# Optimization experiments

Measured on AMD Instinct MI355X. Metric: run time of the kernel, lower is better.

The kernel has to match this reference:

```python
import jax, jax.numpy as jnp
import numpy as np
from jax import lax

D_MODEL = 1024
D_STATE = 16


def setup_inputs() -> dict:
    key = jax.random.key(0)
    ks = jax.random.split(key, 7)
    B, L = 4, 2048
    x = jax.random.normal(ks[0], (B, L, D_MODEL), dtype=jnp.float32)
    s = 1.0 / np.sqrt(D_MODEL)
    W_dt = jax.random.uniform(ks[1], (D_MODEL, D_MODEL), jnp.float32, -s, s)
    b_dt = jax.random.uniform(ks[2], (D_MODEL,), jnp.float32, -s, s)
    W_B = jax.random.uniform(ks[3], (D_STATE, D_MODEL), jnp.float32, -s, s)
    W_C = jax.random.uniform(ks[4], (D_STATE, D_MODEL), jnp.float32, -s, s)
    A = jax.random.normal(ks[5], (D_MODEL, D_STATE), dtype=jnp.float32)
    A_log = jnp.log(jnp.abs(A) + 1e-4)
    D = jnp.ones((D_MODEL,), dtype=jnp.float32)
    return {"x": x, "W_dt": W_dt, "b_dt": b_dt, "W_B": W_B, "W_C": W_C,
            "A_log": A_log, "D": D}


def reference(x, W_dt, b_dt, W_B, W_C, A_log, D):
    B, L, Dm = x.shape
    N = A_log.shape[1]
    dt = jax.nn.softplus(jnp.einsum('bld,ed->ble', x, W_dt) + b_dt)  # [B,L,D]
    Bp = jnp.einsum('bld,nd->bln', x, W_B)   # [B,L,N]
    Cp = jnp.einsum('bld,nd->bln', x, W_C)   # [B,L,N]
    A = -jnp.exp(A_log)                      # [D,N]
    dA = jnp.exp(dt[..., None] * A)          # [B,L,D,N]
    # fuse dB * x: dB[bldn] = dt*Bp; input term = dB * x
    dBx = dt[..., None] * Bp[:, :, None, :] * x[..., None]  # [B,L,D,N]

    def step(h, inp):
        dA_t, dBx_t, C_t, x_t = inp
        h = dA_t * h + dBx_t                              # [B,D,N]
        y = jnp.einsum('bdn,bn->bd', h, C_t) + D * x_t    # [B,D]
        return h, y

    h0 = jnp.zeros((B, Dm, N), dtype=x.dtype)
    xs = (jnp.swapaxes(dA, 0, 1), jnp.swapaxes(dBx, 0, 1),
          jnp.swapaxes(Cp, 0, 1), jnp.swapaxes(x, 0, 1))
    _, ys = lax.scan(step, h0, xs)           # ys: [L,B,D]
    return jnp.swapaxes(ys, 0, 1)            # [B,L,D]
```

## Files before the change

### kernel.cpp

```cpp
#include <hip/hip_runtime.h>
#include <hip/hip_bf16.h>
#include <math.h>

#define DM 1024
#define DS 16
#define BB 4
#define LL 2048
#define LC 32
#define NC (LL/LC)
#define MT 8192
#define NT64 16
#define NCT 17

typedef __attribute__((ext_vector_type(8))) short short8;
typedef __attribute__((ext_vector_type(4))) short short4v;
typedef __attribute__((ext_vector_type(4))) float floatx4;

__device__ __forceinline__ float softplus_fast(float v) {
  return fmaxf(v, 0.f) + __logf(1.f + __expf(-fabsf(v)));
}
__device__ __forceinline__ float bf2f(short s) {
  union { short s2[2]; float f; } u; u.s2[0] = 0; u.s2[1] = s; return u.f;
}

__global__ __launch_bounds__(256) void convert_kernel(
    const float* __restrict__ X, const float* __restrict__ W_dt,
    const float* __restrict__ WB, const float* __restrict__ WC,
    __hip_bfloat16* __restrict__ Xb, __hip_bfloat16* __restrict__ XbT,
    __hip_bfloat16* __restrict__ Wx)
{
  const int tid = threadIdx.x;
  if (blockIdx.x < 2048) {
    __shared__ __hip_bfloat16 tile[64 * 65];
    const int tb = blockIdx.x;
    const int t0 = (tb & 127) * 64;
    const int d0 = (tb >> 7) * 64;
    const int tr  = tid >> 4;
    const int tc4 = (tid & 15) * 4;
#pragma unroll
    for (int p = 0; p < 4; ++p) {
      const int row = p * 16 + tr;
      const float4 v = *(const float4*)&X[(size_t)(t0 + row) * DM + d0 + tc4];
      union { short4v v4; __hip_bfloat16 h[4]; } pk;
      pk.h[0] = __float2bfloat16(v.x); pk.h[1] = __float2bfloat16(v.y);
      pk.h[2] = __float2bfloat16(v.z); pk.h[3] = __float2bfloat16(v.w);
      tile[row * 65 + tc4 + 0] = pk.h[0];
      tile[row * 65 + tc4 + 1] = pk.h[1];
      tile[row * 65 + tc4 + 2] = pk.h[2];
      tile[row * 65 + tc4 + 3] = pk.h[3];
      *(short4v*)&Xb[(size_t)(t0 + row) * DM + d0 + tc4] = pk.v4;
    }
    __syncthreads();
#pragma unroll
    for (int p = 0; p < 4; ++p) {
      const int drow = p * 16 + tr;
      union { short4v v4; __hip_bfloat16 h[4]; } pk;
#pragma unroll
      for (int q = 0; q < 4; ++q)
        pk.h[q] = tile[(tc4 + q) * 65 + drow];
      *(short4v*)&XbT[(size_t)(d0 + drow) * MT + t0 + tc4] = pk.v4;
    }
    return;
  }
  const size_t u0 = (size_t)(blockIdx.x - 2048) * 256 + tid;
  const size_t NW = (size_t)DM * DM / 8;
  const size_t NB = (size_t)DS * DM / 8;
  const float* src;
  __hip_bfloat16* dst;
  size_t u;
  if (u0 < NW)           { src = W_dt; dst = Wx;                       u = u0; }
  else if (u0 < NW + NB) { src = WB;   dst = Wx + (size_t)1024 * DM;   u = u0 - NW; }
  else if (u0 < NW + 2 * NB) { src = WC; dst = Wx + (size_t)1040 * DM; u = u0 - NW - NB; }
  else {
    const size_t z = u0 - NW - 2 * NB;
    const short8 zz = {0, 0, 0, 0, 0, 0, 0, 0};
    *(short8*)&Wx[(size_t)1056 * DM + z * 8] = zz;
    return;
  }
  const float4 a = *(const float4*)&src[u * 8];
  const float4 b = *(const float4*)&src[u * 8 + 4];
  union { short8 v; __hip_bfloat16 h[8]; } o;
  o.h[0] = __float2bfloat16(a.x); o.h[1] = __float2bfloat16(a.y);
  o.h[2] = __float2bfloat16(a.z); o.h[3] = __float2bfloat16(a.w);
  o.h[4] = __float2bfloat16(b.x); o.h[5] = __float2bfloat16(b.y);
  o.h[6] = __float2bfloat16(b.z); o.h[7] = __float2bfloat16(b.w);
  *(short8*)&dst[u * 8] = o.v;
}

__global__ __launch_bounds__(512, 4) void gemm_dt_mfma(
    const __hip_bfloat16* __restrict__ Xb, const __hip_bfloat16* __restrict__ Wx,
    const float* __restrict__ bias, __hip_bfloat16* __restrict__ DTt,
    float* __restrict__ BP, float* __restrict__ CP)
{
  __shared__ short As[2][256 * 64];
  __shared__ short Bs[2][64 * 64];
  const int tid  = threadIdx.x;
  const int lane = tid & 63;
  const int wid  = tid >> 6;
  const int wm   = wid >> 1, wn = wid & 1;

  const int bid  = blockIdx.x;
  const int tile = (bid & 7) * 68 + (bid >> 3);
  const int row0 = (tile / NCT) * 256;
  const int col0 = (tile % NCT) * 64;

  const floatx4 zero = {0.f, 0.f, 0.f, 0.f};
  floatx4 acc[4][2];
#pragma unroll
  for (int i = 0; i < 4; ++i)
#pragma unroll
    for (int j = 0; j < 2; ++j) acc[i][j] = zero;

  auto STAGE = [&](int buf, int t) {
    const int k0 = t * 64;
#pragma unroll
    for (int q = 0; q < 4; ++q) {
      const int fe = q * 512 + tid;
      const int r  = fe >> 3;
      const int kk = (fe & 7) ^ (r & 7);
      __builtin_amdgcn_global_load_lds(
          (const __attribute__((address_space(1))) void*)&Xb[(size_t)(row0 + r) * DM + k0 + kk * 8],
          (__attribute__((address_space(3))) void*)&As[buf][fe * 8], 16, 0, 0);
    }
    {
      const int fe = tid;
      const int r  = fe >> 3;
      const int kk = (fe & 7) ^ (r & 7);
      __builtin_amdgcn_global_load_lds(
          (const __attribute__((address_space(1))) void*)&Wx[(size_t)(col0 + r) * DM + k0 + kk * 8],
          (__attribute__((address_space(3))) void*)&Bs[buf][fe * 8], 16, 0, 0);
    }
  };

  const int fr = lane & 15;
  const int ks = lane >> 4;

  STAGE(0, 0);
  int cur = 0;
  for (int t = 0; t < NT64; ++t) {
    if (t + 1 < NT64) {
      STAGE(cur ^ 1, t + 1);
      asm volatile("s_waitcnt vmcnt(5)" ::: "memory");
    } else {
      asm volatile("s_waitcnt vmcnt(0)" ::: "memory");
    }
    __builtin_amdgcn_s_barrier();
    __builtin_amdgcn_sched_barrier(0);

    short8 af[4][2], bfr[2][2];
#pragma unroll
    for (int i = 0; i < 4; ++i) {
      const int ar = wm * 64 + i * 16 + fr;
#pragma unroll
      for (int s = 0; s < 2; ++s) {
        const int ch = (ks + 4 * s) ^ (ar & 7);
        af[i][s] = *(const short8*)&As[cur][ar * 64 + ch * 8];
      }
    }
#pragma unroll
    for (int j = 0; j < 2; ++j) {
      const int br = wn * 32 + j * 16 + fr;
#pragma unroll
      for (int s = 0; s < 2; ++s) {
        const int ch = (ks + 4 * s) ^ (br & 7);
        bfr[j][s] = *(const short8*)&Bs[cur][br * 64 + ch * 8];
      }
    }
    __builtin_amdgcn_s_setprio(1);
#pragma unroll
    for (int s = 0; s < 2; ++s)
#pragma unroll
      for (int i = 0; i < 4; ++i)
#pragma unroll
        for (int j = 0; j < 2; ++j)
          acc[i][j] = __builtin_amdgcn_mfma_f32_16x16x32_bf16(af[i][s], bfr[j][s], acc[i][j], 0, 0, 0);
    __builtin_amdgcn_s_setprio(0);
    __builtin_amdgcn_sched_barrier(0);

    if (t + 1 < NT64) {
      __builtin_amdgcn_s_barrier();
      cur ^= 1;
    }
  }

  const int cl = lane & 15;
  const int rg = lane >> 4;
  if (col0 < 1024) {
#pragma unroll
    for (int i = 0; i < 4; ++i) {
      const size_t rowbase = (size_t)(row0 + wm * 64 + i * 16 + rg * 4);
#pragma unroll
      for (int j = 0; j < 2; ++j) {
        const int col = col0 + wn * 32 + j * 16 + cl;
        union { short4v v4; __hip_bfloat16 h[4]; } pk;
#pragma unroll
        for (int r = 0; r < 4; ++r)
          pk.h[r] = __float2bfloat16(softplus_fast(acc[i][j][r] + bias[col]));
        *(short4v*)&DTt[(size_t)col * MT + rowbase] = pk.v4;
      }
    }
  } else if (wn == 0) {
#pragma unroll
    for (int i = 0; i < 4; ++i) {
#pragma unroll
      for (int r = 0; r < 4; ++r) {
        const size_t row = (size_t)(row0 + wm * 64 + i * 16 + rg * 4 + r);
        BP[row * DS + cl] = acc[i][0][r];
        CP[row * DS + cl] = acc[i][1][r];
      }
    }
  }
}

__global__ __launch_bounds__(256) void scan_partial_kernel(
    const __hip_bfloat16* __restrict__ DTt, const __hip_bfloat16* __restrict__ XbT,
    const float* __restrict__ Bp, const float* __restrict__ A_log,
    float* __restrict__ SD, __hip_bfloat16* __restrict__ HP)
{
  __shared__ float sB[LC * DS];
  const int tid = threadIdx.x;
  const int d  = blockIdx.x * 128 + (tid >> 1);
  const int nh = tid & 1;
  const int c = blockIdx.y;
  const int b = blockIdx.z;
  const int l0 = c * LC;

  if (tid < LC * DS / 4)
    ((float4*)sB)[tid] = ((const float4*)&Bp[((size_t)b * LL + l0) * DS])[tid];

  float A[8], h[8];
  float sdt = 0.f;
  const float4* arow = (const float4*)&A_log[(size_t)d * DS + nh * 8];
  {
    const float4 a0 = arow[0], a1 = arow[1];
    A[0]=-__expf(a0.x); A[1]=-__expf(a0.y); A[2]=-__expf(a0.z); A[3]=-__expf(a0.w);
    A[4]=-__expf(a1.x); A[5]=-__expf(a1.y); A[6]=-__expf(a1.z); A[7]=-__expf(a1.w);
  }
#pragma unroll
  for (int n = 0; n < 8; ++n) h[n] = 0.f;

  const __hip_bfloat16* dT = &DTt[(size_t)d * MT + (size_t)b * LL + l0];
  const __hip_bfloat16* xT = &XbT[(size_t)d * MT + (size_t)b * LL + l0];
  short8 d8 = *(const short8*)dT;
  short8 x8 = *(const short8*)xT;
  __syncthreads();

  for (int l = 0; l < LC; l += 8) {
    short8 d8n, x8n;
    if (l + 8 < LC) {
      d8n = *(const short8*)(dT + l + 8);
      x8n = *(const short8*)(xT + l + 8);
    }
#pragma unroll
    for (int u = 0; u < 8; ++u) {
      const float dtv = bf2f(d8[u]), xv = bf2f(x8[u]);
      const float dx = dtv * xv;
      sdt += dtv;
      const float4 b0 = ((const float4*)sB)[(l+u)*4 + nh*2 + 0];
      const float4 b1 = ((const float4*)sB)[(l+u)*4 + nh*2 + 1];
      const float bb[8] = {b0.x,b0.y,b0.z,b0.w, b1.x,b1.y,b1.z,b1.w};
#pragma unroll
      for (int n = 0; n < 8; ++n) {
        const float dA = __expf(dtv * A[n]);
        h[n] = fmaf(dA, h[n], dx * bb[n]);
      }
    }
    d8 = d8n; x8 = x8n;
  }
  if (nh == 0) SD[((size_t)b * NC + c) * DM + d] = sdt;
  const size_t o = (((size_t)b * NC + c) * DM + d) * DS + nh * 8;
  union { short8 v; __hip_bfloat16 h[8]; } pk;
#pragma unroll
  for (int n = 0; n < 8; ++n) pk.h[n] = __float2bfloat16(h[n]);
  *(short8*)&HP[o] = pk.v;
}

__global__ __launch_bounds__(256) void combine_kernel(
    const float* __restrict__ SD, const float* __restrict__ A_log,
    __hip_bfloat16* HP)
{
  const int idx = blockIdx.x * 256 + threadIdx.x;
  const int b  = idx >> 14;
  const int dn = idx & 16383;
  const int d  = dn >> 4;
  const float A = -__expf(A_log[dn]);
  float h = 0.f;
#pragma unroll 4
  for (int c = 0; c < NC; ++c) {
    const size_t o = (((size_t)b * NC + c) << 14) + dn;
    const float p  = __expf(SD[((size_t)b * NC + c) * DM + d] * A);
    const float hp = __bfloat162float(HP[o]);
    HP[o] = __float2bfloat16(h);
    h = fmaf(p, h, hp);
  }
}

__global__ __launch_bounds__(256) void scan_final_kernel(
    const __hip_bfloat16* __restrict__ DTt, const __hip_bfloat16* __restrict__ XbT,
    const float* __restrict__ Bp, const float* __restrict__ Cp,
    const float* __restrict__ A_log, const float* __restrict__ Dvec,
    const __hip_bfloat16* __restrict__ Hin, float* __restrict__ Y)
{
  __shared__ float sB[LC * DS], sC[LC * DS];
  const int tid = threadIdx.x;
  const int d  = blockIdx.x * 128 + (tid >> 1);
  const int nh = tid & 1;
  const int c = blockIdx.y;
  const int b = blockIdx.z;
  const int l0 = c * LC;

  if (tid < 128)  ((float4*)sB)[tid] = ((const float4*)&Bp[((size_t)b * LL + l0) * DS])[tid];
  else            ((float4*)sC)[tid - 128] = ((const float4*)&Cp[((size_t)b * LL + l0) * DS])[tid - 128];

  float A[8], h[8];
  const float4* arow = (const float4*)&A_log[(size_t)d * DS + nh * 8];
  {
    const float4 a0 = arow[0], a1 = arow[1];
    A[0]=-__expf(a0.x); A[1]=-__expf(a0.y); A[2]=-__expf(a0.z); A[3]=-__expf(a0.w);
    A[4]=-__expf(a1.x); A[5]=-__expf(a1.y); A[6]=-__expf(a1.z); A[7]=-__expf(a1.w);
  }
  const size_t o = (((size_t)b * NC + c) * DM + d) * DS + nh * 8;
  {
    const short8 hv = *(const short8*)&Hin[o];
#pragma unroll
    for (int n = 0; n < 8; ++n) h[n] = bf2f(hv[n]);
  }
  const float Dd = Dvec[d];
  const size_t tok0 = (size_t)b * LL + l0;
  const __hip_bfloat16* dT = &DTt[(size_t)d * MT + tok0];
  const __hip_bfloat16* xT = &XbT[(size_t)d * MT + tok0];
  short8 d8 = *(const short8*)dT;
  short8 x8 = *(const short8*)xT;
  __syncthreads();

  for (int l = 0; l < LC; l += 8) {
    short8 d8n, x8n;
    if (l + 8 < LC) {
      d8n = *(const short8*)(dT + l + 8);
      x8n = *(const short8*)(xT + l + 8);
    }
#pragma unroll
    for (int u = 0; u < 8; ++u) {
      const float dtv = bf2f(d8[u]), xv = bf2f(x8[u]);
      const float dx = dtv * xv;
      const float4 b0 = ((const float4*)sB)[(l+u)*4 + nh*2 + 0];
      const float4 b1 = ((const float4*)sB)[(l+u)*4 + nh*2 + 1];
      const float bb[8] = {b0.x,b0.y,b0.z,b0.w, b1.x,b1.y,b1.z,b1.w};
      const float4 c0 = ((const float4*)sC)[(l+u)*4 + nh*2 + 0];
      const float4 c1 = ((const float4*)sC)[(l+u)*4 + nh*2 + 1];
      const float cc[8] = {c0.x,c0.y,c0.z,c0.w, c1.x,c1.y,c1.z,c1.w};
      float y = 0.f;
#pragma unroll
      for (int n = 0; n < 8; ++n) {
        const float dA = __expf(dtv * A[n]);
        h[n] = fmaf(dA, h[n], dx * bb[n]);
        y = fmaf(h[n], cc[n], y);
      }
      y += __shfl_xor(y, 1, 64);
      if (nh == 0) Y[(tok0 + l + u) * DM + d] = fmaf(Dd, xv, y);
    }
    d8 = d8n; x8 = x8n;
  }
}

extern "C" void kernel_launch(void* const* d_in, const int* in_sizes, int n_in,
                              void* d_out, int out_size, void* d_ws, size_t ws_size,
                              hipStream_t stream)
{
  const float* x     = (const float*)d_in[0];
  const float* W_dt  = (const float*)d_in[1];
  const float* b_dt  = (const float*)d_in[2];
  const float* W_B   = (const float*)d_in[3];
  const float* W_C   = (const float*)d_in[4];
  const float* A_log = (const float*)d_in[5];
  const float* Dv    = (const float*)d_in[6];
  float* Y  = (float*)d_out;
  float* ws = (float*)d_ws;

  __hip_bfloat16* DTt = (__hip_bfloat16*)ws;
  float* BP = ws + (size_t)MT * DM / 2;
  float* CP = BP + (size_t)MT * DS;
  __hip_bfloat16* Xb  = (__hip_bfloat16*)(CP + (size_t)MT * DS);
  __hip_bfloat16* XbT = Xb + (size_t)MT * DM;
  __hip_bfloat16* Wx  = XbT + (size_t)MT * DM;
  float* SD = (float*)(Wx + (size_t)1088 * DM);
  __hip_bfloat16* HP = (__hip_bfloat16*)(SD + (size_t)BB * NC * DM);

  convert_kernel<<<2592, 256, 0, stream>>>(x, W_dt, W_B, W_C, Xb, XbT, Wx);
  gemm_dt_mfma<<<544, 512, 0, stream>>>(Xb, Wx, b_dt, DTt, BP, CP);
  scan_partial_kernel<<<dim3(DM * 2 / 256, NC, BB), 256, 0, stream>>>(DTt, XbT, BP, A_log, SD, HP);
  combine_kernel<<<(BB * DM * DS) / 256, 256, 0, stream>>>(SD, A_log, HP);
  scan_final_kernel<<<dim3(DM * 2 / 256, NC, BB), 256, 0, stream>>>(DTt, XbT, BP, CP, A_log, Dv, HP, Y);
}
```

Baseline: 119.1 us.

## Fold B/C projection into dt GEMM tiles via split-K atomics

Removes the extra 17th column tile that computed the B and C projections. Each of the 16 dt column tiles now computes one 64-wide K-slice of the B/C projection using the A fragments it already holds, and accumulates the partial results into BP/CP with atomicAdd after a memset. This cuts the grid from 544 to 512 blocks so it matches the CU count more evenly, and drops the zero-padding work in the convert kernel. In exchange it adds a memset launch, many float atomics, and a non-deterministic summation order.

```diff
diff --git a/kernel.cpp b/kernel.cpp
--- a/kernel.cpp
+++ b/kernel.cpp
@@ -10,7 +10,6 @@
 #define NC (LL/LC)
 #define MT 8192
 #define NT64 16
-#define NCT 17
 
 typedef __attribute__((ext_vector_type(8))) short short8;
 typedef __attribute__((ext_vector_type(4))) short short4v;
@@ -68,15 +67,10 @@
   const float* src;
   __hip_bfloat16* dst;
   size_t u;
-  if (u0 < NW)           { src = W_dt; dst = Wx;                       u = u0; }
-  else if (u0 < NW + NB) { src = WB;   dst = Wx + (size_t)1024 * DM;   u = u0 - NW; }
-  else if (u0 < NW + 2 * NB) { src = WC; dst = Wx + (size_t)1040 * DM; u = u0 - NW - NB; }
-  else {
-    const size_t z = u0 - NW - 2 * NB;
-    const short8 zz = {0, 0, 0, 0, 0, 0, 0, 0};
-    *(short8*)&Wx[(size_t)1056 * DM + z * 8] = zz;
-    return;
-  }
+  if (u0 < NW)               { src = W_dt; dst = Wx;                       u = u0; }
+  else if (u0 < NW + NB)     { src = WB;   dst = Wx + (size_t)1024 * DM;   u = u0 - NW; }
+  else if (u0 < NW + 2 * NB) { src = WC;   dst = Wx + (size_t)1040 * DM;   u = u0 - NW - NB; }
+  else return;
   const float4 a = *(const float4*)&src[u * 8];
   const float4 b = *(const float4*)&src[u * 8 + 4];
   union { short8 v; __hip_bfloat16 h[8]; } o;
@@ -100,9 +94,10 @@
   const int wm   = wid >> 1, wn = wid & 1;
 
   const int bid  = blockIdx.x;
-  const int tile = (bid & 7) * 68 + (bid >> 3);
-  const int row0 = (tile / NCT) * 256;
-  const int col0 = (tile % NCT) * 64;
+  const int tile = (bid & 7) * 64 + (bid >> 3);
+  const int row0 = (tile >> 4) * 256;
+  const int ct   = tile & 15;
+  const int col0 = ct * 64;
 
   const floatx4 zero = {0.f, 0.f, 0.f, 0.f};
   floatx4 acc[4][2];
@@ -110,6 +105,9 @@
   for (int i = 0; i < 4; ++i)
 #pragma unroll
     for (int j = 0; j < 2; ++j) acc[i][j] = zero;
+  floatx4 acc_bc[4];
+#pragma unroll
+  for (int i = 0; i < 4; ++i) acc_bc[i] = zero;
 
   auto STAGE = [&](int buf, int t) {
     const int k0 = t * 64;
@@ -135,7 +133,13 @@
   const int fr = lane & 15;
   const int ks = lane >> 4;
 
+  const size_t bcrow = (size_t)(1024 + wn * 16 + fr) * DM + ct * 64 + ks * 8;
+  short8 bc0, bc1;
+
   STAGE(0, 0);
+  bc0 = *(const short8*)&Wx[bcrow];
+  bc1 = *(const short8*)&Wx[bcrow + 32];
+
   int cur = 0;
   for (int t = 0; t < NT64; ++t) {
     if (t + 1 < NT64) {
@@ -175,6 +179,13 @@
         for (int j = 0; j < 2; ++j)
           acc[i][j] = __builtin_amdgcn_mfma_f32_16x16x32_bf16(af[i][s], bfr[j][s], acc[i][j], 0, 0, 0);
     __builtin_amdgcn_s_setprio(0);
+    if (t == ct) {
+#pragma unroll
+      for (int i = 0; i < 4; ++i) {
+        acc_bc[i] = __builtin_amdgcn_mfma_f32_16x16x32_bf16(af[i][0], bc0, acc_bc[i], 0, 0, 0);
+        acc_bc[i] = __builtin_amdgcn_mfma_f32_16x16x32_bf16(af[i][1], bc1, acc_bc[i], 0, 0, 0);
+      }
+    }
     __builtin_amdgcn_sched_barrier(0);
 
     if (t + 1 < NT64) {
@@ -185,29 +196,26 @@
 
   const int cl = lane & 15;
   const int rg = lane >> 4;
-  if (col0 < 1024) {
-#pragma unroll
-    for (int i = 0; i < 4; ++i) {
-      const size_t rowbase = (size_t)(row0 + wm * 64 + i * 16 + rg * 4);
-#pragma unroll
-      for (int j = 0; j < 2; ++j) {
-        const int col = col0 + wn * 32 + j * 16 + cl;
-        union { short4v v4; __hip_bfloat16 h[4]; } pk;
-#pragma unroll
-        for (int r = 0; r < 4; ++r)
-          pk.h[r] = __float2bfloat16(softplus_fast(acc[i][j][r] + bias[col]));
-        *(short4v*)&DTt[(size_t)col * MT + rowbase] = pk.v4;
-      }
-    }
-  } else if (wn == 0) {
-#pragma unroll
-    for (int i = 0; i < 4; ++i) {
-#pragma unroll
-      for (int r = 0; r < 4; ++r) {
-        const size_t row = (size_t)(row0 + wm * 64 + i * 16 + rg * 4 + r);
-        BP[row * DS + cl] = acc[i][0][r];
-        CP[row * DS + cl] = acc[i][1][r];
-      }
+#pragma unroll
+  for (int i = 0; i < 4; ++i) {
+    const size_t rowbase = (size_t)(row0 + wm * 64 + i * 16 + rg * 4);
+#pragma unroll
+    for (int j = 0; j < 2; ++j) {
+      const int col = col0 + wn * 32 + j * 16 + cl;
+      union { short4v v4; __hip_bfloat16 h[4]; } pk;
+#pragma unroll
+      for (int r = 0; r < 4; ++r)
+        pk.h[r] = __float2bfloat16(softplus_fast(acc[i][j][r] + bias[col]));
+      *(short4v*)&DTt[(size_t)col * MT + rowbase] = pk.v4;
+    }
+  }
+  float* dstBC = (wn == 0) ? BP : CP;
+#pragma unroll
+  for (int i = 0; i < 4; ++i) {
+#pragma unroll
+    for (int r = 0; r < 4; ++r) {
+      const size_t row = (size_t)(row0 + wm * 64 + i * 16 + rg * 4 + r);
+      atomicAdd(&dstBC[row * DS + cl], acc_bc[i][r]);
     }
   }
 }
@@ -386,8 +394,9 @@
   float* SD = (float*)(Wx + (size_t)1088 * DM);
   __hip_bfloat16* HP = (__hip_bfloat16*)(SD + (size_t)BB * NC * DM);
 
-  convert_kernel<<<2592, 256, 0, stream>>>(x, W_dt, W_B, W_C, Xb, XbT, Wx);
-  gemm_dt_mfma<<<544, 512, 0, stream>>>(Xb, Wx, b_dt, DTt, BP, CP);
+  hipMemsetAsync(BP, 0, (size_t)2 * MT * DS * sizeof(float), stream);
+  convert_kernel<<<2576, 256, 0, stream>>>(x, W_dt, W_B, W_C, Xb, XbT, Wx);
+  gemm_dt_mfma<<<512, 512, 0, stream>>>(Xb, Wx, b_dt, DTt, BP, CP);
   scan_partial_kernel<<<dim3(DM * 2 / 256, NC, BB), 256, 0, stream>>>(DTt, XbT, BP, A_log, SD, HP);
   combine_kernel<<<(BB * DM * DS) / 256, 256, 0, stream>>>(SD, A_log, HP);
   scan_final_kernel<<<dim3(DM * 2 / 256, NC, BB), 256, 0, stream>>>(DTt, XbT, BP, CP, A_log, Dv, HP, Y);
```

Result: slower. 125.4 us (+5.3%).
